# Optimization experiments

Measured on AMD Instinct MI355X. Metric: run time of the kernel, lower is better.

## Reference

```python
import jax, jax.numpy as jnp
import numpy as np
from jax import lax

RATIOS = (0.5, 1.0, 2.0)
SCALES = (8, 16, 32)
STRIDE = 16
N_ANCHOR = 9
N_PRE = 6000      # eval-mode n_pre_nms
N_POST = 300      # eval-mode n_post_nms
NMS_THRESH = 0.7
MIN_SIZE = 16.0


def _anchor_base():
    rows = []
    for r in RATIOS:
        for s in SCALES:
            h = STRIDE * s * np.sqrt(r)
            w = STRIDE * s * np.sqrt(1.0 / r)
            c = STRIDE / 2.0
            rows.append([c - h / 2.0, c - w / 2.0, c + h / 2.0, c + w / 2.0])
    return jnp.asarray(np.array(rows, np.float32))  # [9,4]


def _all_anchors(hh, ww):
    ab = _anchor_base()
    sy, sx = jnp.meshgrid(jnp.arange(hh) * STRIDE, jnp.arange(ww) * STRIDE, indexing='ij')
    shift = jnp.stack([sy.ravel(), sx.ravel(), sy.ravel(), sx.ravel()], axis=1).astype(jnp.float32)
    return (shift[:, None, :] + ab[None, :, :]).reshape(-1, 4)  # [hh*ww*9, 4]


def _conv(x, w, b, pad):
    y = lax.conv_general_dilated(x, w, (1, 1), ((pad, pad), (pad, pad)),
                                 dimension_numbers=('NCHW', 'OIHW', 'NCHW'))
    return y + b[None, :, None, None]


def _loc2bbox(anchor, loc):
    ah = anchor[:, 2] - anchor[:, 0]
    aw = anchor[:, 3] - anchor[:, 1]
    acy = anchor[:, 0] + 0.5 * ah
    acx = anchor[:, 1] + 0.5 * aw
    dy, dx, dh, dw = loc[:, 0], loc[:, 1], loc[:, 2], loc[:, 3]
    cy = dy * ah + acy
    cx = dx * aw + acx
    h = jnp.exp(dh) * ah
    w = jnp.exp(dw) * aw
    return jnp.stack([cy - 0.5 * h, cx - 0.5 * w, cy + 0.5 * h, cx + 0.5 * w], axis=1)


def _iou_matrix(boxes):
    tl = jnp.maximum(boxes[:, None, :2], boxes[None, :, :2])
    br = jnp.minimum(boxes[:, None, 2:], boxes[None, :, 2:])
    wh = jnp.clip(br - tl, 0.0)
    inter = wh[..., 0] * wh[..., 1]
    area = (boxes[:, 2] - boxes[:, 0]) * (boxes[:, 3] - boxes[:, 1])
    return inter / (area[:, None] + area[None, :] - inter + 1e-9)


def _nms_keep(boxes, valid):
    # boxes sorted by descending score; sequential greedy NMS via fori_loop.
    iou = _iou_matrix(boxes)
    idx = jnp.arange(boxes.shape[0])

    def body(i, keep):
        sup = keep[i] & (iou[i] > NMS_THRESH) & (idx > i)
        return keep & ~sup

    return lax.fori_loop(0, boxes.shape[0], body, valid)


def _proposals(loc, fg_score, anchors, img_h, img_w):
    boxes = _loc2bbox(anchors, loc)
    boxes = jnp.clip(boxes, 0.0, jnp.array([img_h, img_w, img_h, img_w], jnp.float32))
    hs = boxes[:, 2] - boxes[:, 0]
    ws = boxes[:, 3] - boxes[:, 1]
    valid = (hs >= MIN_SIZE) & (ws >= MIN_SIZE)
    score = jnp.where(valid, fg_score, -jnp.inf)
    topv, topi = lax.top_k(score, N_PRE)          # pre-NMS selection by score
    boxes = boxes[topi]
    keep = _nms_keep(boxes, topv > -jnp.inf)
    # compact first N_POST kept boxes (score order), zero-padded if fewer.
    rank = jnp.cumsum(keep) - 1
    pos = jnp.where(keep & (rank < N_POST), rank, N_POST)
    return jnp.zeros((N_POST + 1, 4), boxes.dtype).at[pos].set(boxes)[:N_POST]


def setup_inputs():
    key = jax.random.key(0)
    ks = jax.random.split(key, 4)
    C = 512
    return {
        'feature_map': jax.random.normal(ks[0], (2, C, 64, 64), jnp.float32),
        'conv1_w': jax.random.normal(ks[1], (C, C, 3, 3), jnp.float32) * 0.01,
        'conv1_b': jnp.zeros((C,), jnp.float32),
        'score_w': jax.random.normal(ks[2], (N_ANCHOR * 2, C, 1, 1), jnp.float32) * 0.01,
        'score_b': jnp.zeros((N_ANCHOR * 2,), jnp.float32),
        'loc_w': jax.random.normal(ks[3], (N_ANCHOR * 4, C, 1, 1), jnp.float32) * 0.01,
        'loc_b': jnp.zeros((N_ANCHOR * 4,), jnp.float32),
        'img_h': 1024,
        'img_w': 1024,
    }


def reference(feature_map, conv1_w, conv1_b, score_w, score_b, loc_w, loc_b, img_h, img_w):
    n, _, hh, ww = feature_map.shape
    h = jax.nn.relu(_conv(feature_map, conv1_w, conv1_b, 1))
    rpn_locs = _conv(h, loc_w, loc_b, 0).transpose(0, 2, 3, 1).reshape(n, -1, 4)
    scores_raw = _conv(h, score_w, score_b, 0).transpose(0, 2, 3, 1)  # [n,hh,ww,18]
    sm = jax.nn.softmax(scores_raw.reshape(n, hh, ww, N_ANCHOR, 2), axis=4)
    rpn_fg_scores = sm[..., 1].reshape(n, -1)
    rpn_scores = scores_raw.reshape(n, -1, 2)
    anchors = _all_anchors(hh, ww)
    rois = jax.vmap(lambda l, s: _proposals(l, s, anchors, img_h, img_w))(rpn_locs, rpn_fg_scores)
    roi_indices = jnp.repeat(jnp.arange(n, dtype=jnp.int32), N_POST)
    return rpn_locs, rpn_scores, rois.reshape(-1, 4), roi_indices, anchors
```

## Files before the change

### kernel.cpp

```cpp
#include <hip/hip_runtime.h>
#include <cmath>

#define NANCH 36864
#define NPRE 6000
#define NPOST 300

#define LOCS_OFF   0
#define SCORES_OFF 294912
#define ROIS_OFF   442368
#define RIDX_OFF   444768
#define ANCH_OFF   445368

#define WT_OFF      0ull
#define WTH_OFF     0ull
#define WTL_OFF     4718592ull
#define PREFIX_OFF  2097152ull
#define PREFIXM_OFF 2621440ull
#define SORTED_OFF  3145728ull
#define MASK_OFF    0ull
#define H_OFF       9437184ull
#define BOXES_OFF   26214400ull
#define W54_OFF     26214400ull
#define KEYS_OFF    27394048ull
#define HIST_OFF    27983872ull
#define SKEYS_OFF   28631168ull
#define SBOXES_OFF  28727168ull
#define VMASK_OFF   29033856ull
#define XTH_OFF     29360128ull
#define XTL_OFF     37748736ull
#define WS_NEED_MFMA 46137344ull

typedef _Float16 half8 __attribute__((ext_vector_type(8)));
typedef float floatx4 __attribute__((ext_vector_type(4)));

__device__ __forceinline__ void load_lds16(const float* g, float* l) {
#if __has_builtin(__builtin_amdgcn_global_load_lds)
  __builtin_amdgcn_global_load_lds(
      (const __attribute__((address_space(1))) void*)g,
      (__attribute__((address_space(3))) void*)l, 16, 0, 0);
#else
  int lane = threadIdx.x & 63;
  float4 v = *(const float4*)g;
  *(float4*)((char*)l + lane * 16) = v;
#endif
}

__device__ __forceinline__ void load_lds16g(const void* g, void* l) {
#if __has_builtin(__builtin_amdgcn_global_load_lds)
  __builtin_amdgcn_global_load_lds(
      (const __attribute__((address_space(1))) void*)g,
      (__attribute__((address_space(3))) void*)l, 16, 0, 0);
#else
  int lane = threadIdx.x & 63;
  float4 v = *(const float4*)g;
  *(float4*)((char*)l + lane * 16) = v;
#endif
}

__global__ __launch_bounds__(1024) void prep_kernel(
    const float* __restrict__ w, float* __restrict__ wt,
    const float* __restrict__ lw, const float* __restrict__ sw,
    float* __restrict__ w54p) {
  __shared__ float lds[9][32][33];
  if (blockIdx.x < 256) {
    int tx = threadIdx.x & 31;
    int ty = threadIdx.x >> 5;
    int ci0 = (blockIdx.x & 15) * 32;
    int co0 = (blockIdx.x >> 4) * 32;
    const float* src = w + ((size_t)(co0 + ty) * 512 + (ci0 + tx)) * 9;
#pragma unroll
    for (int k = 0; k < 9; k++) lds[k][tx][ty] = src[k];
    __syncthreads();
#pragma unroll
    for (int k = 0; k < 9; k++) {
      wt[((size_t)k * 512 + (ci0 + ty)) * 512 + co0 + tx] = lds[k][ty][tx];
    }
  } else {
    int t = (blockIdx.x - 256) * 1024 + threadIdx.x;
    int k = t >> 6, co = t & 63;
    float v = 0.f;
    if (co < 36) v = lw[(size_t)co * 512 + k];
    else if (co < 54) v = sw[(size_t)(co - 36) * 512 + k];
    w54p[t] = v;
  }
}

__global__ __launch_bounds__(1024) void prep16_kernel(
    const float* __restrict__ w, _Float16* __restrict__ wth,
    _Float16* __restrict__ wtl, const float* __restrict__ lw,
    const float* __restrict__ sw, float* __restrict__ w54p) {
  if (blockIdx.x < 256) {
    int tx = threadIdx.x & 31;
    int ty = threadIdx.x >> 5;
    int ci0 = (blockIdx.x & 15) * 32;
    int co0 = (blockIdx.x >> 4) * 32;
    const float* src = w + ((size_t)(co0 + ty) * 512 + (ci0 + tx)) * 9;
    size_t o = (size_t)(co0 + ty) * 512 + (ci0 + tx);
#pragma unroll
    for (int k = 0; k < 9; k++) {
      float v = src[k];
      _Float16 h = (_Float16)v;
      _Float16 l = (_Float16)((v - (float)h) * 1024.f);
      wth[(size_t)k * 262144 + o] = h;
      wtl[(size_t)k * 262144 + o] = l;
    }
  } else {
    int t = (blockIdx.x - 256) * 1024 + threadIdx.x;
    int k = t >> 6, co = t & 63;
    float v = 0.f;
    if (co < 36) v = lw[(size_t)co * 512 + k];
    else if (co < 54) v = sw[(size_t)(co - 36) * 512 + k];
    w54p[t] = v;
  }
}

__global__ __launch_bounds__(256) void prepx_kernel(
    const float* __restrict__ x, _Float16* __restrict__ xth,
    _Float16* __restrict__ xtl) {
  __shared__ float xs[32][65];
  int b = blockIdx.x;
  int cs = b & 15, ny = b >> 4;
  int n = ny >> 6, y = ny & 63;
  int tid = threadIdx.x;
  const float* xb = x + ((size_t)n << 21) + (y << 6);
#pragma unroll
  for (int p = 0; p < 8; p++) {
    int c = p * 4 + (tid >> 6);
    xs[c][tid & 63] = xb[((size_t)(cs * 32 + c) << 12) + (tid & 63)];
  }
  __syncthreads();
  int px = tid >> 2, cq = (tid & 3) * 8;
  unsigned int hw[4], lw2[4];
#pragma unroll
  for (int j = 0; j < 4; j++) {
    float v0 = xs[cq + 2 * j][px], v1 = xs[cq + 2 * j + 1][px];
    _Float16 h0 = (_Float16)v0, h1 = (_Float16)v1;
    _Float16 l0 = (_Float16)((v0 - (float)h0) * 1024.f);
    _Float16 l1 = (_Float16)((v1 - (float)h1) * 1024.f);
    hw[j] = (unsigned int)__builtin_bit_cast(unsigned short, h0) |
            ((unsigned int)__builtin_bit_cast(unsigned short, h1) << 16);
    lw2[j] = (unsigned int)__builtin_bit_cast(unsigned short, l0) |
             ((unsigned int)__builtin_bit_cast(unsigned short, l1) << 16);
  }
  size_t o = (size_t)b * 2048 + (size_t)px * 32 + cq;
  uint4 hv; hv.x = hw[0]; hv.y = hw[1]; hv.z = hw[2]; hv.w = hw[3];
  uint4 lv; lv.x = lw2[0]; lv.y = lw2[1]; lv.z = lw2[2]; lv.w = lw2[3];
  *(uint4*)(xth + o) = hv;
  *(uint4*)(xtl + o) = lv;
}

__global__ __launch_bounds__(256, 3) void conv1_mfma_kernel(
    const _Float16* __restrict__ xth, const _Float16* __restrict__ xtl,
    const _Float16* __restrict__ wth, const _Float16* __restrict__ wtl,
    const float* __restrict__ bias, float* __restrict__ hout) {
  __shared__ __align__(16) _Float16 sXh[6336];
  __shared__ __align__(16) _Float16 sXl[6336];
  __shared__ __align__(16) _Float16 sWh[4096];
  __shared__ __align__(16) _Float16 sWl[4096];
  int mb = blockIdx.x;
  int n = mb >> 6, y = mb & 63;
  int co0 = blockIdx.y << 7;
  int tid = threadIdx.x;
  int wv = tid >> 6, lane = tid & 63;
  int m15 = lane & 15, g = lane >> 4;

  floatx4 accm[2][4], accl[2][4];
#pragma unroll
  for (int ct = 0; ct < 2; ct++)
#pragma unroll
    for (int pt = 0; pt < 4; pt++) {
      accm[ct][pt] = (floatx4){0.f, 0.f, 0.f, 0.f};
      accl[ct][pt] = (floatx4){0.f, 0.f, 0.f, 0.f};
    }

  for (int t2 = tid; t2 < 3168; t2 += 256) {
    ((unsigned int*)sXh)[t2] = 0u;
    ((unsigned int*)sXl)[t2] = 0u;
  }
  __syncthreads();

  bool yv0 = (y > 0), yv2 = (y < 63);

  for (int cs = 0; cs < 16; cs++) {
    {
      int base = wv * 6;
#pragma unroll
      for (int i = 0; i < 6; i++) {
        int idx = base + i;
        int yr = idx >> 3, rem = idx & 7;
        int part = rem >> 2, d = rem & 3;
        int ys = y + yr - 1;
        if (ys >= 0 && ys < 64) {
          const _Float16* s =
              (part ? xtl : xth) +
              ((((size_t)(n * 64 + ys)) * 16 + cs) << 11) + (d << 9) +
              ((lane >> 2) << 5) + ((lane & 3) << 3);
          _Float16* dst = (part ? sXl : sXh) + yr * 2112 + 32 + (d << 9);
          load_lds16g(s, dst);
        }
      }
    }
    int ci0 = cs << 5;
    int p = wv >> 1, hf = wv & 1;
    const _Float16* wbase =
        (p ? wtl : wth) + (size_t)co0 * 512 + ci0 +
        ((size_t)(hf * 64 + (lane >> 2))) * 512 + ((lane & 3) << 3);
    _Float16* wdst0 = (p ? sWl : sWh) + (hf << 11);
#pragma unroll
    for (int tap = 0; tap < 9; tap++) {
      int ky = tap / 3;
      int kx = tap - ky * 3;
      if (ky == 0 && !yv0) continue;
      if (ky == 2 && !yv2) continue;
      const _Float16* ws = wbase + (size_t)tap * 262144;
#pragma unroll
      for (int d = 0; d < 4; d++)
        load_lds16g(ws + (size_t)d * 8192, wdst0 + (d << 9));
      __syncthreads();
      half8 Ah[2], Al[2], Bh[4], Bl[4];
#pragma unroll
      for (int ct = 0; ct < 2; ct++) {
        int ao = ((wv << 5) + (ct << 4) + m15) * 32 + (g << 3);
        Ah[ct] = *(const half8*)(sWh + ao);
        Al[ct] = *(const half8*)(sWl + ao);
      }
#pragma unroll
      for (int pt = 0; pt < 4; pt++) {
        int bo = ky * 2112 + ((pt << 4) + m15 + kx) * 32 + (g << 3);
        Bh[pt] = *(const half8*)(sXh + bo);
        Bl[pt] = *(const half8*)(sXl + bo);
      }
#pragma unroll
      for (int ct = 0; ct < 2; ct++)
#pragma unroll
        for (int pt = 0; pt < 4; pt++) {
          accm[ct][pt] = __builtin_amdgcn_mfma_f32_16x16x32_f16(
              Ah[ct], Bh[pt], accm[ct][pt], 0, 0, 0);
          accl[ct][pt] = __builtin_amdgcn_mfma_f32_16x16x32_f16(
              Ah[ct], Bl[pt], accl[ct][pt], 0, 0, 0);
          accl[ct][pt] = __builtin_amdgcn_mfma_f32_16x16x32_f16(
              Al[ct], Bh[pt], accl[ct][pt], 0, 0, 0);
        }
      __syncthreads();
    }
  }

#pragma unroll
  for (int ct = 0; ct < 2; ct++)
#pragma unroll
    for (int pt = 0; pt < 4; pt++) {
#pragma unroll
      for (int r = 0; r < 4; r++) {
        int co = co0 + (wv << 5) + (ct << 4) + (g << 2) + r;
        float v = accm[ct][pt][r] + accl[ct][pt][r] * 0.0009765625f +
                  bias[co];
        hout[((size_t)(n * 512 + co) << 12) + (y << 6) + (pt << 4) + m15] =
            fmaxf(v, 0.f);
      }
    }
}

__global__ __launch_bounds__(256) void conv1_kernel(
    const float* __restrict__ x, const float* __restrict__ wt,
    const float* __restrict__ bias, float* __restrict__ hout) {
  __shared__ __align__(16) float smem[10752];
  int mb = blockIdx.x;
  int n = mb >> 6, y = mb & 63;
  int co0 = blockIdx.y << 7;
  int tid = threadIdx.x;
  int team = tid >> 7;
  int tl = tid & 127;
  int cibase = team << 8;
  float* Asb = smem + team * 768;
  float* Bsb = smem + 1536 + team * 4608;
  int tx = tl & 7, ty = tl >> 3;
  int x0 = tx << 3;

  float acc[8][8];
#pragma unroll
  for (int j = 0; j < 8; j++)
#pragma unroll
    for (int i = 0; i < 8; i++) acc[j][i] = 0.f;

  const float* xb = x + ((size_t)n << 21);

  if (y == 0) {
    for (int t2 = tl; t2 < 256; t2 += 128) Asb[t2] = 0.f;
  }
  if (y == 63) {
    for (int t2 = tl; t2 < 256; t2 += 128) Asb[512 + t2] = 0.f;
  }

  int wv = tl >> 6;
  int lane = tl & 63;
  int lrow = lane >> 5;
  int lcol = (lane & 31) << 2;
  int aci = lane >> 4;
  int aoff = (lane & 15) << 2;

  for (int cc = 0; cc < 256; cc += 4) {
    int ci0 = cibase + cc;
    for (int yr = wv; yr < 3; yr += 2) {
      int ys = y + yr - 1;
      if (ys >= 0 && ys < 64) {
        const float* g =
            xb + (((size_t)(ci0 + aci)) << 12) + (ys << 6) + aoff;
        load_lds16(g, &Asb[yr << 8]);
      }
    }
    for (int i = 0; i < 9; i++) {
      int r0 = i * 4 + wv * 2;
      int row = r0 + lrow;
      int kk = row >> 2, ci = row & 3;
      const float* g = wt + (((size_t)(kk << 9)) + ci0 + ci) * 512 + co0 + lcol;
      load_lds16(g, &Bsb[r0 << 7]);
    }
    __syncthreads();
    for (int k = 0; k < 4; k++) {
#pragma unroll
      for (int ky = 0; ky < 3; ky++) {
        const float* arr = &Asb[((ky << 2) + k) << 6];
        float w10[10];
        w10[0] = (tx == 0) ? 0.f : arr[x0 - 1];
        float4 a0 = *(const float4*)&arr[x0];
        float4 a1 = *(const float4*)&arr[x0 + 4];
        w10[1] = a0.x; w10[2] = a0.y; w10[3] = a0.z; w10[4] = a0.w;
        w10[5] = a1.x; w10[6] = a1.y; w10[7] = a1.z; w10[8] = a1.w;
        w10[9] = (tx == 7) ? 0.f : arr[x0 + 8];
#pragma unroll
        for (int kx = 0; kx < 3; kx++) {
          int kk = ky * 3 + kx;
          const float* br = &Bsb[(((kk << 2) + k) << 7) + (ty << 3)];
          float4 b0 = *(const float4*)br;
          float4 b1 = *(const float4*)(br + 4);
          float bb[8] = {b0.x, b0.y, b0.z, b0.w, b1.x, b1.y, b1.z, b1.w};
#pragma unroll
          for (int j = 0; j < 8; j++)
#pragma unroll
            for (int dx = 0; dx < 8; dx++)
              acc[j][dx] = fmaf(w10[kx + dx], bb[j], acc[j][dx]);
        }
      }
    }
    __syncthreads();
  }

  if (team == 1) {
#pragma unroll
    for (int j = 0; j < 8; j++) {
      *(float4*)&smem[tl * 68 + (j << 3)] = *(float4*)&acc[j][0];
      *(float4*)&smem[tl * 68 + (j << 3) + 4] = *(float4*)&acc[j][4];
    }
  }
  __syncthreads();
  if (team == 0) {
#pragma unroll
    for (int j = 0; j < 8; j++) {
      int co = co0 + (ty << 3) + j;
      float bv = bias[co];
      float4 p0 = *(float4*)&smem[tl * 68 + (j << 3)];
      float4 p1 = *(float4*)&smem[tl * 68 + (j << 3) + 4];
      float4 v0, v1;
      v0.x = fmaxf((acc[j][0] + p0.x) + bv, 0.f);
      v0.y = fmaxf((acc[j][1] + p0.y) + bv, 0.f);
      v0.z = fmaxf((acc[j][2] + p0.z) + bv, 0.f);
      v0.w = fmaxf((acc[j][3] + p0.w) + bv, 0.f);
      v1.x = fmaxf((acc[j][4] + p1.x) + bv, 0.f);
      v1.y = fmaxf((acc[j][5] + p1.y) + bv, 0.f);
      v1.z = fmaxf((acc[j][6] + p1.z) + bv, 0.f);
      v1.w = fmaxf((acc[j][7] + p1.w) + bv, 0.f);
      float* o = &hout[(((size_t)(n * 512 + co)) << 12) + (y << 6) + x0];
      *(float4*)o = v0;
      *(float4*)(o + 4) = v1;
    }
  }
}

__global__ __launch_bounds__(256) void heads_kernel(
    const float* __restrict__ h, const float* __restrict__ w54p,
    const float* __restrict__ loc_b, const float* __restrict__ score_b,
    float* __restrict__ out) {
  __shared__ __align__(16) float hs[32 * 64];
  __shared__ __align__(16) float wsd[32 * 64];
  __shared__ float sacc[64 * 65];
  int n = blockIdx.x >> 6;
  int p0 = (blockIdx.x & 63) << 6;
  int tid = threadIdx.x;
  int txp = tid & 63;
  int tw = tid >> 6;
  float acc[16];
#pragma unroll
  for (int j = 0; j < 16; j++) acc[j] = 0.f;
  const float* hb = h + ((size_t)n * 512) * 4096 + p0;
  for (int k0 = 0; k0 < 512; k0 += 32) {
    for (int t = tid; t < 512; t += 256) {
      int r = t >> 4, l = (t & 15) << 2;
      *(float4*)&hs[(r << 6) + l] =
          *(const float4*)&hb[(((size_t)(k0 + r)) << 12) + l];
      *(float4*)&wsd[(r << 6) + l] =
          *(const float4*)&w54p[((k0 + r) << 6) + l];
    }
    __syncthreads();
    for (int k = 0; k < 32; k++) {
      float hv = hs[(k << 6) + txp];
      const float* wr = &wsd[(k << 6) + (tw << 4)];
#pragma unroll
      for (int u = 0; u < 4; u++) {
        float4 wv = *(const float4*)(wr + (u << 2));
        acc[u * 4 + 0] = fmaf(hv, wv.x, acc[u * 4 + 0]);
        acc[u * 4 + 1] = fmaf(hv, wv.y, acc[u * 4 + 1]);
        acc[u * 4 + 2] = fmaf(hv, wv.z, acc[u * 4 + 2]);
        acc[u * 4 + 3] = fmaf(hv, wv.w, acc[u * 4 + 3]);
      }
    }
    __syncthreads();
  }
#pragma unroll
  for (int j = 0; j < 16; j++) sacc[(tw * 16 + j) * 65 + txp] = acc[j];
  __syncthreads();
  for (int t = tid; t < 64 * 54; t += 256) {
    int p = t / 54, c = t - p * 54;
    float v = sacc[c * 65 + p];
    int gp = (n << 12) + p0 + p;
    if (c < 36) out[LOCS_OFF + (size_t)gp * 36 + c] = v + loc_b[c];
    else out[SCORES_OFF + (size_t)gp * 18 + (c - 36)] = v + score_b[c - 36];
  }
}

__global__ void decode_kernel(const float* __restrict__ out_ro,
                              const int* __restrict__ pimh,
                              const int* __restrict__ pimw,
                              float* __restrict__ boxes,
                              unsigned long long* __restrict__ keys,
                              unsigned int* __restrict__ hist,
                              float* __restrict__ out) {
  int t = blockIdx.x * 256 + threadIdx.x;
  int n = t / NANCH, k = t - n * NANCH;
  float imh = (float)pimh[0], imw = (float)pimw[0];

  int a = k % 9, pos = k / 9;
  int jj = pos & 63, ii = pos >> 6;
  int ridx = a / 3, sidx = a % 3;
  double r = (ridx == 0) ? 0.5 : ((ridx == 1) ? 1.0 : 2.0);
  double s = (sidx == 0) ? 8.0 : ((sidx == 1) ? 16.0 : 32.0);
  double ahh = 16.0 * s * sqrt(r);
  double aww = 16.0 * s * sqrt(1.0 / r);
  float b0 = (float)(8.0 - ahh / 2.0), b1 = (float)(8.0 - aww / 2.0);
  float b2 = (float)(8.0 + ahh / 2.0), b3 = (float)(8.0 + aww / 2.0);
  float sy = (float)(ii * 16), sx = (float)(jj * 16);
  float a0 = sy + b0, a1 = sx + b1, a2 = sy + b2, a3 = sx + b3;
  if (n == 0) {
    float* o = out + ANCH_OFF + (size_t)k * 4;
    o[0] = a0; o[1] = a1; o[2] = a2; o[3] = a3;
  }

  const float* loc = out_ro + LOCS_OFF + (size_t)t * 4;
  const float* sc = out_ro + SCORES_OFF + (size_t)t * 2;
  float ah = __fsub_rn(a2, a0), aw = __fsub_rn(a3, a1);
  float acy = __fadd_rn(a0, 0.5f * ah), acx = __fadd_rn(a1, 0.5f * aw);
  float dy = loc[0], dx = loc[1], dh = loc[2], dw = loc[3];
  float cy = __fadd_rn(__fmul_rn(dy, ah), acy);
  float cx = __fadd_rn(__fmul_rn(dx, aw), acx);
  float hh = __fmul_rn(expf(dh), ah);
  float ww = __fmul_rn(expf(dw), aw);
  float y1 = __fsub_rn(cy, 0.5f * hh), x1 = __fsub_rn(cx, 0.5f * ww);
  float y2 = __fadd_rn(cy, 0.5f * hh), x2 = __fadd_rn(cx, 0.5f * ww);
  y1 = fminf(fmaxf(y1, 0.f), imh); x1 = fminf(fmaxf(x1, 0.f), imw);
  y2 = fminf(fmaxf(y2, 0.f), imh); x2 = fminf(fmaxf(x2, 0.f), imw);
  bool valid = (__fsub_rn(y2, y1) >= 16.f) && (__fsub_rn(x2, x1) >= 16.f);
  float s0 = sc[0], s1 = sc[1];
  float m = fmaxf(s0, s1);
  float e0 = expf(__fsub_rn(s0, m)), e1 = expf(__fsub_rn(s1, m));
  float fg = __fdiv_rn(e1, __fadd_rn(e0, e1));
  float score = valid ? fg : -INFINITY;
  unsigned int u = __float_as_uint(score);
  unsigned int ord = (u & 0x80000000u) ? ~u : (u | 0x80000000u);
  unsigned long long key =
      ((unsigned long long)(~ord) << 16) | (unsigned long long)(k & 0xFFFF);
  float4 b4; b4.x = y1; b4.y = x1; b4.z = y2; b4.w = x2;
  *(float4*)(boxes + (size_t)t * 4) = b4;
  keys[t] = key;
  if (valid)
    atomicAdd(&hist[((size_t)n << 16) + (unsigned int)(key >> 32)], 1u);
}

__global__ __launch_bounds__(1024) void scanfull_kernel(
    const unsigned int* __restrict__ hist, unsigned int* __restrict__ prefix,
    unsigned int* __restrict__ prefix_mut) {
  int n = blockIdx.x;
  const uint4* h4 = (const uint4*)(hist + ((size_t)n << 16));
  uint4* pf4 = (uint4*)(prefix + ((size_t)n << 16));
  uint4* pm4 = (uint4*)(prefix_mut + ((size_t)n << 16));
  __shared__ unsigned int ps[1024];
  int tid = threadIdx.x;
  int base4 = tid << 4;
  uint4 vals[16];
  unsigned int s = 0;
#pragma unroll
  for (int i = 0; i < 16; i++) {
    vals[i] = h4[base4 + i];
    s += vals[i].x + vals[i].y + vals[i].z + vals[i].w;
  }
  ps[tid] = s;
  __syncthreads();
  for (int off = 1; off < 1024; off <<= 1) {
    unsigned int v = ps[tid];
    unsigned int add = (tid >= off) ? ps[tid - off] : 0u;
    __syncthreads();
    ps[tid] = v + add;
    __syncthreads();
  }
  unsigned int run = ps[tid] - s;
#pragma unroll
  for (int i = 0; i < 16; i++) {
    uint4 hv = vals[i];
    uint4 pv;
    pv.x = run; run += hv.x;
    pv.y = run; run += hv.y;
    pv.z = run; run += hv.z;
    pv.w = run; run += hv.w;
    pf4[base4 + i] = pv;
    pm4[base4 + i] = pv;
  }
}

__global__ void scatter_kernel(const unsigned long long* __restrict__ keys,
                               unsigned int* __restrict__ prefix_mut,
                               unsigned long long* __restrict__ sorted) {
  int t = blockIdx.x * 256 + threadIdx.x;
  int n = t / NANCH;
  unsigned long long key = keys[t];
  unsigned int b = (unsigned int)(key >> 32);
  if (b >= 0xFF80u) return;
  unsigned int pos = atomicAdd(&prefix_mut[((size_t)n << 16) + b], 1u);
  if (pos < 8192) sorted[((size_t)n << 13) + pos] = key;
}

__global__ void fixup_kernel(const unsigned long long* __restrict__ sorted,
                             const unsigned int* __restrict__ prefix,
                             const unsigned int* __restrict__ hist,
                             const float* __restrict__ boxes,
                             unsigned long long* __restrict__ skeys,
                             float* __restrict__ sboxes) {
  int t = blockIdx.x * 256 + threadIdx.x;
  int n = t / 7168;
  int s = t - n * 7168;
  const unsigned long long* srt = sorted + ((size_t)n << 13);
  unsigned long long key = srt[s];
  unsigned int hi = (unsigned int)(key >> 16);
  if (hi >= 0xFF800000u) {
    if (s < NPRE) skeys[(size_t)n * NPRE + s] = key;
    return;
  }
  unsigned int b = (unsigned int)(key >> 32);
  unsigned int st = prefix[((size_t)n << 16) + b];
  if (st >= (unsigned)NPRE) return;
  unsigned int cnt = hist[((size_t)n << 16) + b];
  unsigned int r = 0;
  if (cnt > 1) {
    for (unsigned int j = 0; j < cnt; j++) r += (srt[st + j] < key) ? 1u : 0u;
  }
  unsigned int pos = st + r;
  if (pos < (unsigned)NPRE) {
    skeys[(size_t)n * NPRE + pos] = key;
    int k = (int)(key & 0xFFFFull);
    float4 bx = *(const float4*)(boxes + (((size_t)n * NANCH) + k) * 4);
    *(float4*)(sboxes + ((size_t)n * NPRE + pos) * 4) = bx;
  }
}

__global__ __launch_bounds__(64) void nms_mask_kernel(
    const float* __restrict__ sboxes,
    const unsigned long long* __restrict__ skeys,
    unsigned long long* __restrict__ vmask,
    unsigned long long* __restrict__ mask) {
  int n = blockIdx.z;
  int ib = blockIdx.x, jb = blockIdx.y;
  if (jb < ib) return;
  int lane = threadIdx.x;
  __shared__ __align__(16) float jbox[64][4];
  int j = jb * 64 + lane;
  float4 bj4 = (j < NPRE)
                   ? *(const float4*)(sboxes + ((size_t)n * NPRE + j) * 4)
                   : float4{0.f, 0.f, 0.f, 0.f};
  *(float4*)jbox[lane] = bj4;
  __syncthreads();
  if (jb == ib) {
    int idx = ib * 64 + lane;
    bool ok = false;
    if (idx < NPRE) {
      unsigned int khi = (unsigned int)(skeys[(size_t)n * NPRE + idx] >> 16);
      ok = khi < 0xFF800000u;
    }
    unsigned long long m = __ballot(ok);
    if (lane == 0) vmask[(size_t)n * 94 + ib] = m;
  }
  int i = ib * 64 + lane;
  if (i >= NPRE) return;
  float4 bi = *(const float4*)(sboxes + ((size_t)n * NPRE + i) * 4);
  float ay1 = bi.x, ax1 = bi.y, ay2 = bi.z, ax2 = bi.w;
  float areaA = __fmul_rn(__fsub_rn(ay2, ay1), __fsub_rn(ax2, ax1));
  unsigned long long bits = 0ull;
#pragma unroll 8
  for (int l = 0; l < 64; l++) {
    float4 bj = *(const float4*)jbox[l];
    float ty1 = fmaxf(ay1, bj.x), tx1 = fmaxf(ax1, bj.y);
    float ty2 = fminf(ay2, bj.z), tx2 = fminf(ax2, bj.w);
    float wh0 = fmaxf(__fsub_rn(ty2, ty1), 0.f);
    float wh1 = fmaxf(__fsub_rn(tx2, tx1), 0.f);
    float inter = __fmul_rn(wh0, wh1);
    float areaB = __fmul_rn(__fsub_rn(bj.z, bj.x), __fsub_rn(bj.w, bj.y));
    float den = __fadd_rn(__fsub_rn(__fadd_rn(areaA, areaB), inter), 1e-9f);
    float iou = __fdiv_rn(inter, den);
    if (iou > 0.7f) bits |= (1ull << l);
  }
  mask[((size_t)n * NPRE + i) * 94 + jb] = bits;
}

#define WARM_ROWS 2048

__global__ __launch_bounds__(1024) void nms_reduce_kernel(
    const unsigned long long* __restrict__ mask,
    const unsigned long long* __restrict__ vmask,
    const float* __restrict__ sboxes, float* __restrict__ out) {
  int n = blockIdx.x;
  __shared__ int kept[NPOST];

  {
    const ulonglong2* m2 =
        (const ulonglong2*)(mask + (size_t)n * NPRE * 94);
    unsigned long long accw = 0;
    const int total = WARM_ROWS * 94 / 2;
    for (int i = threadIdx.x; i < total; i += 1024) {
      ulonglong2 v = m2[i];
      accw ^= v.x ^ v.y;
    }
    asm volatile("" :: "v"(accw));
  }
  __syncthreads();
  if (threadIdx.x >= 64) return;

  int lane = threadIdx.x;

  unsigned long long rlo = ~vmask[(size_t)n * 94 + lane];
  unsigned long long rhi = (64 + lane < 94) ? ~vmask[(size_t)n * 94 + 64 + lane]
                                            : ~0ull;
  int count = 0;
  for (int c = 0; c < 94 && count < NPOST; c++) {
    unsigned long long curw =
        (c < 64) ? __shfl(rlo, c) : __shfl(rhi, c - 64);
    unsigned long long cand = ~curw;
    while (cand != 0ull && count < NPOST) {
      int b = __builtin_ctzll(cand);
      int i = c * 64 + b;
      if (lane == 0) kept[count] = i;
      count++;
      const unsigned long long* row = mask + ((size_t)n * NPRE + i) * 94;
      unsigned long long r0 = row[lane];
      unsigned long long r1 = (64 + lane < 94) ? row[64 + lane] : 0ull;
      rlo |= r0; rhi |= r1;
      curw = (c < 64) ? __shfl(rlo, c) : __shfl(rhi, c - 64);
      cand = ~curw;
      cand &= (b == 63) ? 0ull : (~0ull << (b + 1));
    }
  }

  float* rois = out + ROIS_OFF + (size_t)n * NPOST * 4;
  float* ridx = out + RIDX_OFF + (size_t)n * NPOST;
  for (int s = lane; s < NPOST; s += 64) {
    float4 v = {0.f, 0.f, 0.f, 0.f};
    if (s < count) {
      int i = kept[s];
      v = *(const float4*)(sboxes + ((size_t)n * NPRE + i) * 4);
    }
    *(float4*)(rois + (size_t)s * 4) = v;
    ridx[s] = (float)n;
  }
}

extern "C" void kernel_launch(void* const* d_in, const int* in_sizes, int n_in,
                              void* d_out, int out_size, void* d_ws,
                              size_t ws_size, hipStream_t stream) {
  const float* feat = (const float*)d_in[0];
  const float* w1 = (const float*)d_in[1];
  const float* b1 = (const float*)d_in[2];
  const float* sw = (const float*)d_in[3];
  const float* sb = (const float*)d_in[4];
  const float* lw = (const float*)d_in[5];
  const float* lb = (const float*)d_in[6];
  const int* pimh = (const int*)d_in[7];
  const int* pimw = (const int*)d_in[8];
  float* out = (float*)d_out;
  char* ws = (char*)d_ws;

  float* wt = (float*)(ws + WT_OFF);
  _Float16* wth = (_Float16*)(ws + WTH_OFF);
  _Float16* wtl = (_Float16*)(ws + WTL_OFF);
  _Float16* xth = (_Float16*)(ws + XTH_OFF);
  _Float16* xtl = (_Float16*)(ws + XTL_OFF);
  float* w54p = (float*)(ws + W54_OFF);
  float* hbuf = (float*)(ws + H_OFF);
  float* boxes = (float*)(ws + BOXES_OFF);
  unsigned long long* keys = (unsigned long long*)(ws + KEYS_OFF);
  unsigned int* hist = (unsigned int*)(ws + HIST_OFF);
  unsigned int* prefix = (unsigned int*)(ws + PREFIX_OFF);
  unsigned int* prefix_mut = (unsigned int*)(ws + PREFIXM_OFF);
  unsigned long long* sorted = (unsigned long long*)(ws + SORTED_OFF);
  unsigned long long* skeys = (unsigned long long*)(ws + SKEYS_OFF);
  float* sboxes = (float*)(ws + SBOXES_OFF);
  unsigned long long* vmask = (unsigned long long*)(ws + VMASK_OFF);
  unsigned long long* nmask = (unsigned long long*)(ws + MASK_OFF);

  hipMemsetAsync(ws + HIST_OFF, 0, 524288, stream);
  hipMemsetAsync(ws + SORTED_OFF, 0xFF, 131072, stream);

  bool big = (ws_size >= WS_NEED_MFMA);
  if (big) {
    prep16_kernel<<<288, 1024, 0, stream>>>(w1, wth, wtl, lw, sw, w54p);
    prepx_kernel<<<2048, 256, 0, stream>>>(feat, xth, xtl);
    conv1_mfma_kernel<<<dim3(128, 4), 256, 0, stream>>>(xth, xtl, wth, wtl,
                                                        b1, hbuf);
  } else {
    prep_kernel<<<288, 1024, 0, stream>>>(w1, wt, lw, sw, w54p);
    conv1_kernel<<<dim3(128, 4), 256, 0, stream>>>(feat, wt, b1, hbuf);
  }
  heads_kernel<<<128, 256, 0, stream>>>(hbuf, w54p, lb, sb, out);
  decode_kernel<<<288, 256, 0, stream>>>(out, pimh, pimw, boxes, keys, hist,
                                         out);
  scanfull_kernel<<<2, 1024, 0, stream>>>(hist, prefix, prefix_mut);
  scatter_kernel<<<288, 256, 0, stream>>>(keys, prefix_mut, sorted);
  fixup_kernel<<<56, 256, 0, stream>>>(sorted, prefix, hist, boxes, skeys,
                                       sboxes);
  nms_mask_kernel<<<dim3(94, 94, 2), 64, 0, stream>>>(sboxes, skeys, vmask,
                                                      nmask);
  nms_reduce_kernel<<<2, 1024, 0, stream>>>(nmask, vmask, sboxes, out);
}
```

Measured before the change: 618.6 us.

## Relayout conv weights and inputs for contiguous LDS loads and prefetch NMS rows

Changes the fp16 hi/lo weight and input packing so each 8-channel group is stored contiguously per output-channel tile and per pixel. The conv kernel can then issue linear global-to-LDS copies and read A/B fragments from a group-major LDS layout with padding, which should cut uncoalesced loads and LDS bank conflicts. Separately, the greedy NMS loop speculatively loads the next candidate's mask row to warm the cache. The speculative loads add memory traffic, and the prefetched row may be suppressed and never used.

After: 662.5 us. 7.1% more time.

```diff
diff --git a/kernel.cpp b/kernel.cpp
--- a/kernel.cpp
+++ b/kernel.cpp
@@ -94,15 +94,20 @@
     int ty = threadIdx.x >> 5;
     int ci0 = (blockIdx.x & 15) * 32;
     int co0 = (blockIdx.x >> 4) * 32;
-    const float* src = w + ((size_t)(co0 + ty) * 512 + (ci0 + tx)) * 9;
-    size_t o = (size_t)(co0 + ty) * 512 + (ci0 + tx);
+    int ci = ci0 + tx, co = co0 + ty;
+    const float* src = w + ((size_t)co * 512 + ci) * 9;
+    int cot = co >> 7, coin = co & 127;
+    int cs = ci >> 5, gg = (ci >> 3) & 3, cii = ci & 7;
+    size_t obase = ((((size_t)cot) * 16 + cs) * 4 + gg) * 1024 +
+                   (size_t)coin * 8 + cii;
 #pragma unroll
     for (int k = 0; k < 9; k++) {
       float v = src[k];
       _Float16 h = (_Float16)v;
       _Float16 l = (_Float16)((v - (float)h) * 1024.f);
-      wth[(size_t)k * 262144 + o] = h;
-      wtl[(size_t)k * 262144 + o] = l;
+      size_t o = (size_t)k * 262144 + obase;
+      wth[o] = h;
+      wtl[o] = l;
     }
   } else {
     int t = (blockIdx.x - 256) * 1024 + threadIdx.x;
@@ -129,11 +134,11 @@
     xs[c][tid & 63] = xb[((size_t)(cs * 32 + c) << 12) + (tid & 63)];
   }
   __syncthreads();
-  int px = tid >> 2, cq = (tid & 3) * 8;
+  int px = tid & 63, gx = tid >> 6;
   unsigned int hw[4], lw2[4];
 #pragma unroll
   for (int j = 0; j < 4; j++) {
-    float v0 = xs[cq + 2 * j][px], v1 = xs[cq + 2 * j + 1][px];
+    float v0 = xs[gx * 8 + 2 * j][px], v1 = xs[gx * 8 + 2 * j + 1][px];
     _Float16 h0 = (_Float16)v0, h1 = (_Float16)v1;
     _Float16 l0 = (_Float16)((v0 - (float)h0) * 1024.f);
     _Float16 l1 = (_Float16)((v1 - (float)h1) * 1024.f);
@@ -142,7 +147,7 @@
     lw2[j] = (unsigned int)__builtin_bit_cast(unsigned short, l0) |
              ((unsigned int)__builtin_bit_cast(unsigned short, l1) << 16);
   }
-  size_t o = (size_t)b * 2048 + (size_t)px * 32 + cq;
+  size_t o = (size_t)b * 2048 + (size_t)gx * 512 + (size_t)px * 8;
   uint4 hv; hv.x = hw[0]; hv.y = hw[1]; hv.z = hw[2]; hv.w = hw[3];
   uint4 lv; lv.x = lw2[0]; lv.y = lw2[1]; lv.z = lw2[2]; lv.w = lw2[3];
   *(uint4*)(xth + o) = hv;
@@ -180,6 +185,9 @@
   __syncthreads();
 
   bool yv0 = (y > 0), yv2 = (y < 63);
+  int p = wv >> 1, hf = wv & 1;
+  _Float16* wdst = p ? sWl : sWh;
+  const _Float16* wsel = p ? wtl : wth;
 
   for (int cs = 0; cs < 16; cs++) {
     {
@@ -194,39 +202,38 @@
           const _Float16* s =
               (part ? xtl : xth) +
               ((((size_t)(n * 64 + ys)) * 16 + cs) << 11) + (d << 9) +
-              ((lane >> 2) << 5) + ((lane & 3) << 3);
-          _Float16* dst = (part ? sXl : sXh) + yr * 2112 + 32 + (d << 9);
+              (lane << 3);
+          _Float16* dst = (part ? sXl : sXh) + yr * 2112 + d * 528 + 8;
           load_lds16g(s, dst);
         }
       }
     }
-    int ci0 = cs << 5;
-    int p = wv >> 1, hf = wv & 1;
-    const _Float16* wbase =
-        (p ? wtl : wth) + (size_t)co0 * 512 + ci0 +
-        ((size_t)(hf * 64 + (lane >> 2))) * 512 + ((lane & 3) << 3);
-    _Float16* wdst0 = (p ? sWl : sWh) + (hf << 11);
+    size_t woff0 = (size_t)(co0 >> 7) * 65536 + (size_t)cs * 4096;
+    const _Float16* wsrc0 = wsel + woff0 + (lane << 3);
 #pragma unroll
     for (int tap = 0; tap < 9; tap++) {
       int ky = tap / 3;
       int kx = tap - ky * 3;
       if (ky == 0 && !yv0) continue;
       if (ky == 2 && !yv2) continue;
-      const _Float16* ws = wbase + (size_t)tap * 262144;
-#pragma unroll
-      for (int d = 0; d < 4; d++)
-        load_lds16g(ws + (size_t)d * 8192, wdst0 + (d << 9));
+      const _Float16* ws = wsrc0 + (size_t)tap * 262144;
+#pragma unroll
+      for (int e = 0; e < 4; e++) {
+        int gd = hf * 2 + (e >> 1), half = e & 1;
+        load_lds16g(ws + gd * 1024 + half * 512,
+                    wdst + gd * 1024 + half * 512);
+      }
       __syncthreads();
       half8 Ah[2], Al[2], Bh[4], Bl[4];
 #pragma unroll
       for (int ct = 0; ct < 2; ct++) {
-        int ao = ((wv << 5) + (ct << 4) + m15) * 32 + (g << 3);
+        int ao = (g << 10) + (((wv << 5) + (ct << 4) + m15) << 3);
         Ah[ct] = *(const half8*)(sWh + ao);
         Al[ct] = *(const half8*)(sWl + ao);
       }
 #pragma unroll
       for (int pt = 0; pt < 4; pt++) {
-        int bo = ky * 2112 + ((pt << 4) + m15 + kx) * 32 + (g << 3);
+        int bo = ky * 2112 + g * 528 + (((pt << 4) + m15 + kx) << 3);
         Bh[pt] = *(const half8*)(sXh + bo);
         Bl[pt] = *(const half8*)(sXl + bo);
       }
@@ -645,6 +652,7 @@
   unsigned long long rlo = ~vmask[(size_t)n * 94 + lane];
   unsigned long long rhi = (64 + lane < 94) ? ~vmask[(size_t)n * 94 + 64 + lane]
                                             : ~0ull;
+  unsigned long long pf = 0;
   int count = 0;
   for (int c = 0; c < 94 && count < NPOST; c++) {
     unsigned long long curw =
@@ -658,12 +666,20 @@
       const unsigned long long* row = mask + ((size_t)n * NPRE + i) * 94;
       unsigned long long r0 = row[lane];
       unsigned long long r1 = (64 + lane < 94) ? row[64 + lane] : 0ull;
+      unsigned long long candr = cand & (cand - 1);
+      if (candr != 0ull) {
+        int ip = c * 64 + (int)__builtin_ctzll(candr);
+        const unsigned long long* rp = mask + ((size_t)n * NPRE + ip) * 94;
+        pf ^= rp[lane];
+        if (64 + lane < 94) pf ^= rp[64 + lane];
+      }
       rlo |= r0; rhi |= r1;
       curw = (c < 64) ? __shfl(rlo, c) : __shfl(rhi, c - 64);
       cand = ~curw;
       cand &= (b == 63) ? 0ull : (~0ull << (b + 1));
     }
   }
+  asm volatile("" :: "v"(pf));
 
   float* rois = out + ROIS_OFF + (size_t)n * NPOST * 4;
   float* ridx = out + RIDX_OFF + (size_t)n * NPOST;
```
